# Performance work log

Hardware: AMD Instinct MI355X
Metric: run time of the kernel (lower is better)

Reference implementation:

```python
import jax, jax.numpy as jnp
import numpy as np

B, S, FEA, T = 32, 8, 2560, 800   # batch, speakers, feature dim (20*128), time frames
N_CLUSTERS, EMB = 512, 256        # speaker-embedding dictionary shape (m)
H = 8                             # n_heads


def setup_inputs() -> dict:
    key = jax.random.key(0)
    ks = jax.random.split(key, 9)
    x = jax.random.normal(ks[0], (B, FEA, T), dtype=jnp.float32)
    mask = jax.random.uniform(ks[1], (B, S, T), dtype=jnp.float32)
    # learned params
    W_w = jax.random.normal(ks[2], (H, FEA), dtype=jnp.float32) * 0.02
    W_b = jnp.zeros((H,), dtype=jnp.float32)
    U_w = jax.random.normal(ks[3], (H, EMB), dtype=jnp.float32) * 0.02
    U_b = jnp.zeros((H,), dtype=jnp.float32)
    v_w = jax.random.normal(ks[4], (1, H), dtype=jnp.float32) * 0.1
    v_b = jnp.zeros((1,), dtype=jnp.float32)
    # speaker-embedding dictionary (self.m loaded from .npy)
    m = jax.random.normal(ks[5], (N_CLUSTERS, EMB), dtype=jnp.float32)
    return {"x": x, "mask": mask, "W_w": W_w, "W_b": W_b,
            "U_w": U_w, "U_b": U_b, "v_w": v_w, "v_b": v_b, "m": m}


def reference(x, mask, W_w, W_b, U_w, U_b, v_w, v_b, m):
    # masked mean-pool over time: (B,S,Fea) -- avoids the torch .repeat blowup
    pooled = jnp.einsum('bft,bst->bsf', x, mask)
    denom = jnp.sum(mask, axis=2)[..., None] + 1e-10   # (B,S,1)
    x2 = pooled / denom                                 # (B,S,Fea)
    # additive attention scores over clusters
    w = x2 @ W_w.T + W_b                                # (B,S,H)
    u = m @ U_w.T + U_b                                 # (N,H)
    s = jnp.tanh(w[:, :, None, :] + u[None, None, :, :])  # (B,S,N,H)
    c = jnp.einsum('bsnh,h->bsn', s, v_w[0]) + v_b[0]   # (B,S,N)
    a = jax.nn.sigmoid(c)
    # gated weighted sum of cluster embeddings
    e = jnp.einsum('bsn,ne->bse', a, m)                 # (B,S,Emb)
    return e
```

## Files before the change

### kernel.cpp

```cpp
#include <hip/hip_runtime.h>
#include <hip/hip_bf16.h>
#include <math.h>

#define B 32
#define S 8
#define FEA 2560
#define T 800
#define NCL 512
#define EMB 256
#define H 8

#define BF 64
#define SEC 128
#define NSEC 6
#define WVB 4096
#define MROWB 1664

typedef __attribute__((ext_vector_type(8))) short bf16x8;
typedef __attribute__((ext_vector_type(4))) float f32x4;

__device__ __forceinline__ short4 cvt_bf16x4(float4 v) {
    union { short4 s4; __hip_bfloat162 h[2]; } u;
    u.h[0] = __float22bfloat162_rn(make_float2(v.x, v.y));
    u.h[1] = __float22bfloat162_rn(make_float2(v.z, v.w));
    return u.s4;
}

__device__ __forceinline__ void load_sec_w(const float* __restrict__ xw, int sec,
                                           int lane, float4 R[8]) {
    const int c4 = lane & 31;
    #pragma unroll
    for (int r = 0; r < 8; ++r) {
        const int row = r * 2 + (lane >> 5);
        R[r] = *(const float4*)(xw + (size_t)row * T + sec * SEC + c4 * 4);
    }
}

__device__ __forceinline__ void write_sec_w(char* __restrict__ buf, int lane, const float4 R[8]) {
    const int c4 = lane & 31;
    #pragma unroll
    for (int r = 0; r < 8; ++r) {
        const int row = r * 2 + (lane >> 5);
        *(short4*)(buf + row * 256 + ((c4 * 8) ^ ((row & 7) << 4))) = cvt_bf16x4(R[r]);
    }
}

#define STEP4(secv, bufp) {                                                          \
    _Pragma("unroll")                                                                \
    for (int st_ = 0; st_ < 4; ++st_) {                                              \
        const bf16x8 bx_ = *(const bf16x8*)((bufp) + xrow * 256                      \
                              + ((st_ * 64 + kb16) ^ xswz));                         \
        const bf16x8 am_ = *(const bf16x8*)((const char*)mask_l + mbase              \
                              + ((((secv) * 4 + st_) * 64 + kb16) ^ mswz));          \
        acc = __builtin_amdgcn_mfma_f32_16x16x32_bf16(am_, bx_, acc, 0, 0, 0);       \
    }                                                                                \
}

__global__ __launch_bounds__(256) void pool_u_kernel(const float* __restrict__ x,
                                                     const float* __restrict__ mask,
                                                     const float* __restrict__ U_w,
                                                     const float* __restrict__ U_b,
                                                     const float* __restrict__ m,
                                                     float* __restrict__ pooled,
                                                     float* __restrict__ u_out) {
    const int b = blockIdx.y;

    if (blockIdx.x == FEA / BF) {
        if (b >= 8) return;
        const int n  = b * 64 + (threadIdx.x >> 2);
        const int h0 = (threadIdx.x & 3) * 2;
        float a0 = 0.f, a1 = 0.f;
        #pragma unroll 4
        for (int e = 0; e < EMB; ++e) {
            const float mv = m[n * EMB + e];
            a0 += mv * U_w[h0 * EMB + e];
            a1 += mv * U_w[(h0 + 1) * EMB + e];
        }
        u_out[n * H + h0]     = a0 + U_b[h0];
        u_out[n * H + h0 + 1] = a1 + U_b[h0 + 1];
        return;
    }

    __shared__ short mask_l[S * (MROWB / 2)];
    __shared__ char  xls[4 * 2 * WVB];

    const int tid  = threadIdx.x;
    const int wave = tid >> 6, lane = tid & 63;
    const int f0   = blockIdx.x * BF;

    const float* xw = x + ((size_t)b * FEA + f0 + wave * 16) * T;
    char* buf0 = xls + wave * 2 * WVB;
    char* buf1 = buf0 + WVB;

    float4 R0[8], R1[8];

    load_sec_w(xw, 0, lane, R0);
    load_sec_w(xw, 1, lane, R1);

    for (int v = tid; v < S * 200; v += 256) {
        const int s = v / 200, c4 = v % 200;
        const float4 mv = *(const float4*)(mask + ((size_t)(b * S + s)) * T + c4 * 4);
        const int byte = s * MROWB + ((c4 * 8) ^ (s << 4));
        *(short4*)((char*)mask_l + byte) = cvt_bf16x4(mv);
    }
    __syncthreads();

    write_sec_w(buf0, lane, R0);
    load_sec_w(xw, 2, lane, R0);
    write_sec_w(buf1, lane, R1);
    load_sec_w(xw, 3, lane, R1);

    const int kb16 = (lane >> 4) * 16;
    const int xrow = lane & 15;
    const int xswz = (xrow & 7) << 4;
    const int srow = lane & 7;
    const int mbase = srow * MROWB;
    const int mswz = srow << 4;

    f32x4 acc = {0.f, 0.f, 0.f, 0.f};

    #pragma unroll 1
    for (int st = 0; st < 4; st += 2) {
        STEP4(st, buf0)
        write_sec_w(buf0, lane, R0);
        if (st + 4 < NSEC) load_sec_w(xw, st + 4, lane, R0);
        STEP4(st + 1, buf1)
        write_sec_w(buf1, lane, R1);
        if (st + 5 < NSEC) load_sec_w(xw, st + 5, lane, R1);
    }
    STEP4(4, buf0)
    STEP4(5, buf1)

    {
        const float* xt = xw + (size_t)xrow * T + 768 + (lane >> 4) * 8;
        const float4 t0 = *(const float4*)(xt);
        const float4 t1 = *(const float4*)(xt + 4);
        union { bf16x8 v; short4 s4[2]; } Bx;
        Bx.s4[0] = cvt_bf16x4(t0);
        Bx.s4[1] = cvt_bf16x4(t1);
        const bf16x8 am = *(const bf16x8*)((const char*)mask_l + mbase
                              + ((24 * 64 + kb16) ^ mswz));
        acc = __builtin_amdgcn_mfma_f32_16x16x32_bf16(am, Bx.v, acc, 0, 0, 0);
    }

    if (lane < 32) {
        const int col = lane & 15;
        #pragma unroll
        for (int i = 0; i < 4; ++i) {
            const int sr = (lane >> 4) * 4 + i;
            pooled[(size_t)(b * S + sr) * FEA + f0 + wave * 16 + col] = acc[i];
        }
    }
}

__global__ __launch_bounds__(256) void wden_kernel(const float* __restrict__ pooled,
                                                   const float* __restrict__ mask,
                                                   const float* __restrict__ W_w,
                                                   const float* __restrict__ W_b,
                                                   float* __restrict__ w_out) {
    __shared__ float red[256];
    __shared__ float wred[4][8];
    const int bs  = blockIdx.x;
    const int tid = threadIdx.x;

    float p = 0.f;
    for (int t = tid; t < T; t += 256) p += mask[(size_t)bs * T + t];
    red[tid] = p;
    __syncthreads();
    for (int st = 128; st > 0; st >>= 1) {
        if (tid < st) red[tid] += red[tid + st];
        __syncthreads();
    }
    const float inv_d = 1.f / (red[0] + 1e-10f);

    float acc[8];
    #pragma unroll
    for (int h = 0; h < 8; ++h) acc[h] = 0.f;
    for (int f = tid; f < FEA; f += 256) {
        const float xv = pooled[(size_t)bs * FEA + f] * inv_d;
        #pragma unroll
        for (int h = 0; h < 8; ++h) acc[h] += xv * W_w[h * FEA + f];
    }
    const int lane = tid & 63, wave = tid >> 6;
    #pragma unroll
    for (int h = 0; h < 8; ++h) {
        float v = acc[h];
        #pragma unroll
        for (int off = 32; off > 0; off >>= 1) v += __shfl_xor(v, off, 64);
        if (lane == 0) wred[wave][h] = v;
    }
    __syncthreads();
    if (tid < 8)
        w_out[bs * H + tid] = wred[0][tid] + wred[1][tid] + wred[2][tid] + wred[3][tid] + W_b[tid];
}

__global__ __launch_bounds__(256) void gate_kernel(const float* __restrict__ w_buf,
                                                   const float* __restrict__ u_buf,
                                                   const float* __restrict__ v_w,
                                                   const float* __restrict__ v_b,
                                                   float* __restrict__ a_out,
                                                   float* __restrict__ out) {
    const int idx = blockIdx.x * 256 + threadIdx.x;
    if (idx < B * S * EMB) out[idx] = 0.f;
    const int bs = idx >> 9, n = idx & 511;
    float c = v_b[0];
    #pragma unroll
    for (int h = 0; h < 8; ++h)
        c += tanhf(w_buf[bs * H + h] + u_buf[n * H + h]) * v_w[h];
    a_out[idx] = 1.f / (1.f + expf(-c));
}

__global__ __launch_bounds__(256) void egemv_kernel(const float* __restrict__ a_buf,
                                                    const float* __restrict__ m,
                                                    float* __restrict__ out) {
    __shared__ float a_sh[256];
    const int bs = blockIdx.x >> 1, half = blockIdx.x & 1;
    const int tid = threadIdx.x;
    a_sh[tid] = a_buf[bs * NCL + half * 256 + tid];
    __syncthreads();
    float acc = 0.f;
    #pragma unroll 8
    for (int n = 0; n < 256; ++n)
        acc += a_sh[n] * m[(half * 256 + n) * EMB + tid];
    atomicAdd(&out[bs * EMB + tid], acc);
}

extern "C" void kernel_launch(void* const* d_in, const int* in_sizes, int n_in,
                              void* d_out, int out_size, void* d_ws, size_t ws_size,
                              hipStream_t stream) {
    const float* x    = (const float*)d_in[0];
    const float* mask = (const float*)d_in[1];
    const float* W_w  = (const float*)d_in[2];
    const float* W_b  = (const float*)d_in[3];
    const float* U_w  = (const float*)d_in[4];
    const float* U_b  = (const float*)d_in[5];
    const float* v_w  = (const float*)d_in[6];
    const float* v_b  = (const float*)d_in[7];
    const float* m    = (const float*)d_in[8];
    float* out = (float*)d_out;

    float* ws     = (float*)d_ws;
    float* pooled = ws;
    float* u_buf  = pooled + B * S * FEA;
    float* w_buf  = u_buf + NCL * H;
    float* a_buf  = w_buf + B * S * H;

    pool_u_kernel<<<dim3(FEA / BF + 1, B), 256, 0, stream>>>(
        x, mask, U_w, U_b, m, pooled, u_buf);
    wden_kernel<<<B * S, 256, 0, stream>>>(pooled, mask, W_w, W_b, w_buf);
    gate_kernel<<<B * S * NCL / 256, 256, 0, stream>>>(w_buf, u_buf, v_w, v_b, a_buf, out);
    egemv_kernel<<<B * S * 2, 256, 0, stream>>>(a_buf, m, out);
}
```

Measured before the change: 75.13 us.

## Load mask fragments directly into registers and fuse gate into egemv kernel

The pooling kernel no longer stages the whole bf16 mask in LDS behind a block barrier. Each lane loads its own mask MFMA fragments straight from global memory, double-buffered alongside the x sections, and the kernel gets a launch_bounds occupancy hint. The sigmoid gate computation moves into the egemv kernel and the output zeroing moves into wden, which removes one kernel launch and the a_buf round trip. The cost is redundant mask reads across the four waves and more register pressure.

```diff
diff --git a/kernel.cpp b/kernel.cpp
--- a/kernel.cpp
+++ b/kernel.cpp
@@ -14,7 +14,6 @@
 #define SEC 128
 #define NSEC 6
 #define WVB 4096
-#define MROWB 1664
 
 typedef __attribute__((ext_vector_type(8))) short bf16x8;
 typedef __attribute__((ext_vector_type(4))) float f32x4;
@@ -45,24 +44,36 @@
     }
 }
 
-#define STEP4(secv, bufp) {                                                          \
+__device__ __forceinline__ void load_mfrag(const float* __restrict__ mrow, int sec,
+                                           int kb, bf16x8 M[4]) {
+    #pragma unroll
+    for (int st = 0; st < 4; ++st) {
+        const float* p = mrow + sec * SEC + st * 32 + kb * 8;
+        const float4 m0 = *(const float4*)(p);
+        const float4 m1 = *(const float4*)(p + 4);
+        union { bf16x8 v; short4 s4[2]; } u;
+        u.s4[0] = cvt_bf16x4(m0);
+        u.s4[1] = cvt_bf16x4(m1);
+        M[st] = u.v;
+    }
+}
+
+#define STEP4(bufp, M) {                                                             \
     _Pragma("unroll")                                                                \
     for (int st_ = 0; st_ < 4; ++st_) {                                              \
         const bf16x8 bx_ = *(const bf16x8*)((bufp) + xrow * 256                      \
                               + ((st_ * 64 + kb16) ^ xswz));                         \
-        const bf16x8 am_ = *(const bf16x8*)((const char*)mask_l + mbase              \
-                              + ((((secv) * 4 + st_) * 64 + kb16) ^ mswz));          \
-        acc = __builtin_amdgcn_mfma_f32_16x16x32_bf16(am_, bx_, acc, 0, 0, 0);       \
+        acc = __builtin_amdgcn_mfma_f32_16x16x32_bf16(M[st_], bx_, acc, 0, 0, 0);    \
     }                                                                                \
 }
 
-__global__ __launch_bounds__(256) void pool_u_kernel(const float* __restrict__ x,
-                                                     const float* __restrict__ mask,
-                                                     const float* __restrict__ U_w,
-                                                     const float* __restrict__ U_b,
-                                                     const float* __restrict__ m,
-                                                     float* __restrict__ pooled,
-                                                     float* __restrict__ u_out) {
+__global__ __launch_bounds__(256, 4) void pool_u_kernel(const float* __restrict__ x,
+                                                        const float* __restrict__ mask,
+                                                        const float* __restrict__ U_w,
+                                                        const float* __restrict__ U_b,
+                                                        const float* __restrict__ m,
+                                                        float* __restrict__ pooled,
+                                                        float* __restrict__ u_out) {
     const int b = blockIdx.y;
 
     if (blockIdx.x == FEA / BF) {
@@ -81,66 +92,64 @@
         return;
     }
 
-    __shared__ short mask_l[S * (MROWB / 2)];
-    __shared__ char  xls[4 * 2 * WVB];
+    __shared__ char xls[4 * 2 * WVB];
 
     const int tid  = threadIdx.x;
     const int wave = tid >> 6, lane = tid & 63;
     const int f0   = blockIdx.x * BF;
 
-    const float* xw = x + ((size_t)b * FEA + f0 + wave * 16) * T;
+    const int kb16 = (lane >> 4) * 16;
+    const int kb   = lane >> 4;
+    const int xrow = lane & 15;
+    const int xswz = (xrow & 7) << 4;
+    const int srow = lane & 7;
+
+    const float* xw   = x + ((size_t)b * FEA + f0 + wave * 16) * T;
+    const float* mrow = mask + ((size_t)(b * S + srow)) * T;
     char* buf0 = xls + wave * 2 * WVB;
     char* buf1 = buf0 + WVB;
 
     float4 R0[8], R1[8];
+    bf16x8 Ma[4], Mb[4];
 
     load_sec_w(xw, 0, lane, R0);
     load_sec_w(xw, 1, lane, R1);
-
-    for (int v = tid; v < S * 200; v += 256) {
-        const int s = v / 200, c4 = v % 200;
-        const float4 mv = *(const float4*)(mask + ((size_t)(b * S + s)) * T + c4 * 4);
-        const int byte = s * MROWB + ((c4 * 8) ^ (s << 4));
-        *(short4*)((char*)mask_l + byte) = cvt_bf16x4(mv);
-    }
-    __syncthreads();
-
+    load_mfrag(mrow, 0, kb, Ma);
     write_sec_w(buf0, lane, R0);
     load_sec_w(xw, 2, lane, R0);
     write_sec_w(buf1, lane, R1);
     load_sec_w(xw, 3, lane, R1);
 
-    const int kb16 = (lane >> 4) * 16;
-    const int xrow = lane & 15;
-    const int xswz = (xrow & 7) << 4;
-    const int srow = lane & 7;
-    const int mbase = srow * MROWB;
-    const int mswz = srow << 4;
-
     f32x4 acc = {0.f, 0.f, 0.f, 0.f};
 
     #pragma unroll 1
-    for (int st = 0; st < 4; st += 2) {
-        STEP4(st, buf0)
-        write_sec_w(buf0, lane, R0);
-        if (st + 4 < NSEC) load_sec_w(xw, st + 4, lane, R0);
-        STEP4(st + 1, buf1)
-        write_sec_w(buf1, lane, R1);
-        if (st + 5 < NSEC) load_sec_w(xw, st + 5, lane, R1);
-    }
-    STEP4(4, buf0)
-    STEP4(5, buf1)
+    for (int st = 0; st < NSEC; st += 2) {
+        load_mfrag(mrow, st + 1, kb, Mb);
+        STEP4(buf0, Ma)
+        if (st + 2 < NSEC) {
+            write_sec_w(buf0, lane, R0);
+            if (st + 4 < NSEC) load_sec_w(xw, st + 4, lane, R0);
+            load_mfrag(mrow, st + 2, kb, Ma);
+        }
+        STEP4(buf1, Mb)
+        if (st + 3 < NSEC) {
+            write_sec_w(buf1, lane, R1);
+            if (st + 5 < NSEC) load_sec_w(xw, st + 5, lane, R1);
+        }
+    }
 
     {
-        const float* xt = xw + (size_t)xrow * T + 768 + (lane >> 4) * 8;
+        const float* xt = xw + (size_t)xrow * T + 768 + kb * 8;
         const float4 t0 = *(const float4*)(xt);
         const float4 t1 = *(const float4*)(xt + 4);
         union { bf16x8 v; short4 s4[2]; } Bx;
         Bx.s4[0] = cvt_bf16x4(t0);
         Bx.s4[1] = cvt_bf16x4(t1);
-        const bf16x8 am = *(const bf16x8*)((const char*)mask_l + mbase
-                              + ((24 * 64 + kb16) ^ mswz));
-        acc = __builtin_amdgcn_mfma_f32_16x16x32_bf16(am, Bx.v, acc, 0, 0, 0);
+        const float* mp = mrow + 768 + kb * 8;
+        union { bf16x8 v; short4 s4[2]; } Am;
+        Am.s4[0] = cvt_bf16x4(*(const float4*)(mp));
+        Am.s4[1] = cvt_bf16x4(*(const float4*)(mp + 4));
+        acc = __builtin_amdgcn_mfma_f32_16x16x32_bf16(Am.v, Bx.v, acc, 0, 0, 0);
     }
 
     if (lane < 32) {
@@ -157,11 +166,14 @@
                                                    const float* __restrict__ mask,
                                                    const float* __restrict__ W_w,
                                                    const float* __restrict__ W_b,
-                                                   float* __restrict__ w_out) {
+                                                   float* __restrict__ w_out,
+                                                   float* __restrict__ out) {
     __shared__ float red[256];
     __shared__ float wred[4][8];
     const int bs  = blockIdx.x;
     const int tid = threadIdx.x;
+
+    out[bs * EMB + tid] = 0.f;
 
     float p = 0.f;
     for (int t = tid; t < T; t += 256) p += mask[(size_t)bs * T + t];
@@ -194,34 +206,28 @@
         w_out[bs * H + tid] = wred[0][tid] + wred[1][tid] + wred[2][tid] + wred[3][tid] + W_b[tid];
 }
 
-__global__ __launch_bounds__(256) void gate_kernel(const float* __restrict__ w_buf,
-                                                   const float* __restrict__ u_buf,
-                                                   const float* __restrict__ v_w,
-                                                   const float* __restrict__ v_b,
-                                                   float* __restrict__ a_out,
-                                                   float* __restrict__ out) {
-    const int idx = blockIdx.x * 256 + threadIdx.x;
-    if (idx < B * S * EMB) out[idx] = 0.f;
-    const int bs = idx >> 9, n = idx & 511;
-    float c = v_b[0];
-    #pragma unroll
-    for (int h = 0; h < 8; ++h)
-        c += tanhf(w_buf[bs * H + h] + u_buf[n * H + h]) * v_w[h];
-    a_out[idx] = 1.f / (1.f + expf(-c));
-}
-
-__global__ __launch_bounds__(256) void egemv_kernel(const float* __restrict__ a_buf,
+__global__ __launch_bounds__(256) void egemv_kernel(const float* __restrict__ w_buf,
+                                                    const float* __restrict__ u_buf,
+                                                    const float* __restrict__ v_w,
+                                                    const float* __restrict__ v_b,
                                                     const float* __restrict__ m,
                                                     float* __restrict__ out) {
     __shared__ float a_sh[256];
     const int bs = blockIdx.x >> 1, half = blockIdx.x & 1;
     const int tid = threadIdx.x;
-    a_sh[tid] = a_buf[bs * NCL + half * 256 + tid];
+    const int n = half * 256 + tid;
+
+    float c = v_b[0];
+    #pragma unroll
+    for (int h = 0; h < 8; ++h)
+        c += tanhf(w_buf[bs * H + h] + u_buf[n * H + h]) * v_w[h];
+    a_sh[tid] = 1.f / (1.f + expf(-c));
     __syncthreads();
+
     float acc = 0.f;
     #pragma unroll 8
-    for (int n = 0; n < 256; ++n)
-        acc += a_sh[n] * m[(half * 256 + n) * EMB + tid];
+    for (int n2 = 0; n2 < 256; ++n2)
+        acc += a_sh[n2] * m[(half * 256 + n2) * EMB + tid];
     atomicAdd(&out[bs * EMB + tid], acc);
 }
 
@@ -243,11 +249,9 @@
     float* pooled = ws;
     float* u_buf  = pooled + B * S * FEA;
     float* w_buf  = u_buf + NCL * H;
-    float* a_buf  = w_buf + B * S * H;
 
     pool_u_kernel<<<dim3(FEA / BF + 1, B), 256, 0, stream>>>(
         x, mask, U_w, U_b, m, pooled, u_buf);
-    wden_kernel<<<B * S, 256, 0, stream>>>(pooled, mask, W_w, W_b, w_buf);
-    gate_kernel<<<B * S * NCL / 256, 256, 0, stream>>>(w_buf, u_buf, v_w, v_b, a_buf, out);
-    egemv_kernel<<<B * S * 2, 256, 0, stream>>>(a_buf, m, out);
-}
+    wden_kernel<<<B * S, 256, 0, stream>>>(pooled, mask, W_w, W_b, w_buf, out);
+    egemv_kernel<<<B * S * 2, 256, 0, stream>>>(w_buf, u_buf, v_w, v_b, m, out);
+}
```

Measured after the change: 134.2 us. 78.6% more time.
